# Kernel optimization log

Hardware: AMD Instinct MI355X
Metric: run time of the kernel (lower is better)

Reference implementation:

```python
import jax, jax.numpy as jnp
import numpy as np

D = 768
H = 12
DH = D // H  # 64


def setup_inputs() -> dict:
    key = jax.random.key(0)
    ks = jax.random.split(key, 7)
    B, N = 16, 1024
    sequences = jax.random.normal(ks[0], (B, N, D), dtype=jnp.float32)
    s = 1.0 / np.sqrt(DH)
    # per-head torch Linear params: weight [out, in] = [DH, DH], bias [DH]
    Wq = jax.random.uniform(ks[1], (H, DH, DH), jnp.float32, -s, s)
    Wk = jax.random.uniform(ks[2], (H, DH, DH), jnp.float32, -s, s)
    Wv = jax.random.uniform(ks[3], (H, DH, DH), jnp.float32, -s, s)
    bq = jax.random.uniform(ks[4], (H, DH), jnp.float32, -s, s)
    bk = jax.random.uniform(ks[5], (H, DH), jnp.float32, -s, s)
    bv = jax.random.uniform(ks[6], (H, DH), jnp.float32, -s, s)
    return {"sequences": sequences, "Wq": Wq, "Wk": Wk, "Wv": Wv,
            "bq": bq, "bk": bk, "bv": bv}


def reference(sequences, Wq, Wk, Wv, bq, bk, bv):
    B, N, _ = sequences.shape
    x = sequences.reshape(B, N, H, DH)  # head slices of the feature dim
    # torch Linear: y = x @ W.T + b  -> einsum over the 'in' axis of W
    q = jnp.einsum('bnhd,hed->bnhe', x, Wq) + bq
    k = jnp.einsum('bnhd,hed->bnhe', x, Wk) + bk
    v = jnp.einsum('bnhd,hed->bnhe', x, Wv) + bv
    scores = jnp.einsum('bnhe,bmhe->bhnm', q, k) / jnp.sqrt(jnp.float32(DH))
    attn = jax.nn.softmax(scores, axis=-1)  # [B,H,N,N]
    out = jnp.einsum('bhnm,bmhe->bnhe', attn, v)
    return out.reshape(B, N, H * DH)  # hstack of per-head outputs
```

## Files before the change

### kernel.cpp

```cpp
#include <hip/hip_runtime.h>


#define NH 12
#define DHEAD 64
#define BB 16
#define NSEQ 1024
#define DMODEL 768
#define LSTR 72
#define QSCALE 0.18033688f

typedef unsigned short u16;
typedef unsigned int u32;
typedef u16 u16x8 __attribute__((ext_vector_type(8)));
typedef u16 u16x4 __attribute__((ext_vector_type(4)));
typedef __bf16 bf16x8 __attribute__((ext_vector_type(8)));
typedef __bf16 bf16x2 __attribute__((ext_vector_type(2)));
typedef float f32x4 __attribute__((ext_vector_type(4)));
typedef int i32x2 __attribute__((ext_vector_type(2)));

union Frag { u16x8 u; bf16x8 b; u32 w[4]; };

__device__ __forceinline__ float fast_exp2(float x) {
#if __has_builtin(__builtin_amdgcn_exp2f)
    return __builtin_amdgcn_exp2f(x);
#else
    return exp2f(x);
#endif
}

__device__ __forceinline__ u16 f2bf(float f) {
    union { __bf16 h; u16 u; } c; c.h = (__bf16)f; return c.u;
}

__device__ __forceinline__ u32 pk2(float lo, float hi) {
    union { bf16x2 b; u32 u; } c;
    c.b[0] = (__bf16)lo; c.b[1] = (__bf16)hi;
    return c.u;
}

__device__ __forceinline__ u16x8 cvt8(const float* __restrict__ p) {
    f32x4 a = *(const f32x4*)p;
    f32x4 b = *(const f32x4*)(p + 4);
    Frag r;
    r.b[0] = (__bf16)a[0]; r.b[1] = (__bf16)a[1]; r.b[2] = (__bf16)a[2]; r.b[3] = (__bf16)a[3];
    r.b[4] = (__bf16)b[0]; r.b[5] = (__bf16)b[1]; r.b[6] = (__bf16)b[2]; r.b[7] = (__bf16)b[3];
    return r.u;
}

__device__ __forceinline__ int sw(int row, int slot) {
    return (row << 6) + (((slot + row) & 7) << 3);
}

__device__ __forceinline__ void lane4_shuffle(u32 a0, u32 a1, u32& wlo, u32& whi) {
    i32x2 t = __builtin_amdgcn_permlane32_swap((int)a0, (int)a1, false, false);
    i32x2 r = __builtin_amdgcn_permlane16_swap(t[0], t[1], false, false);
    wlo = (u32)r[0]; whi = (u32)r[1];
}

__global__ __launch_bounds__(256) void wcvt_kernel(
    const float* __restrict__ Wq, const float* __restrict__ Wk,
    const float* __restrict__ Wv, u16* __restrict__ Wb)
{
    const int bx = blockIdx.x;
    const int m = bx / 24;
    const int off = (bx % 24) * 2048 + threadIdx.x * 8;
    const float* srcs[3] = { Wq, Wk, Wv };
    *(u16x8*)(Wb + m * 49152 + off) = cvt8(srcs[m] + off);
}

__global__ __launch_bounds__(256) void kv_kernel(
    const float* __restrict__ x,
    const u16*  __restrict__ Wb,
    const float* __restrict__ bk, const float* __restrict__ bv,
    u16* __restrict__ Ko,
    u16* __restrict__ Vt)
{
    __shared__ __align__(16) u16 w_lds[2][64 * LSTR];
    __shared__ __align__(16) u16 x_lds[128 * LSTR];

    const int bid = blockIdx.x;
    const int h     = bid % NH;
    const int chunk = (bid / NH) & 7;
    const int b     = bid / (NH * 8);

    const int t = threadIdx.x, lane = t & 63, wave = t >> 6;
    const int qd = lane >> 4, lm = lane & 15;

    {
        const int row = t >> 2, d0 = (t & 3) * 16;
#pragma unroll
        for (int m = 0; m < 2; m++) {
            const u16* s = Wb + (1 + m) * 49152 + h * 4096 + row * 64 + d0;
            *(u16x8*)&w_lds[m][row * LSTR + d0]     = *(const u16x8*)s;
            *(u16x8*)&w_lds[m][row * LSTR + d0 + 8] = *(const u16x8*)(s + 8);
        }
        const int xr = t >> 1, xd = (t & 1) * 32;
        const float* s = x + ((size_t)(b * NSEQ + chunk * 128 + xr)) * DMODEL + h * DHEAD + xd;
#pragma unroll
        for (int i = 0; i < 4; i++)
            *(u16x8*)&x_lds[xr * LSTR + xd + i * 8] = cvt8(s + i * 8);
    }
    __syncthreads();

    Frag xfrag[2][2];
#pragma unroll
    for (int mt = 0; mt < 2; mt++)
#pragma unroll
        for (int kk = 0; kk < 2; kk++)
            xfrag[mt][kk].u = *(const u16x8*)&x_lds[(wave * 32 + mt * 16 + lm) * LSTR + kk * 32 + qd * 8];

    u16* tx = &x_lds[wave * 32 * LSTR];
    const int key_base = chunk * 128 + wave * 32;

#pragma unroll
    for (int et = 0; et < 4; et++) {
        Frag wfrag[2];
#pragma unroll
        for (int kk = 0; kk < 2; kk++)
            wfrag[kk].u = *(const u16x8*)&w_lds[0][(et * 16 + lm) * LSTR + kk * 32 + qd * 8];
        f32x4 acc0 = {0.f,0.f,0.f,0.f}, acc1 = {0.f,0.f,0.f,0.f};
#pragma unroll
        for (int kk = 0; kk < 2; kk++) {
            acc0 = __builtin_amdgcn_mfma_f32_16x16x32_bf16(wfrag[kk].b, xfrag[0][kk].b, acc0, 0, 0, 0);
            acc1 = __builtin_amdgcn_mfma_f32_16x16x32_bf16(wfrag[kk].b, xfrag[1][kk].b, acc1, 0, 0, 0);
        }
        f32x4 b4 = *(const f32x4*)&bk[h * DHEAD + et * 16 + qd * 4];
        u16x4 o0, o1;
#pragma unroll
        for (int r = 0; r < 4; r++) {
            o0[r] = f2bf(acc0[r] + b4[r]);
            o1[r] = f2bf(acc1[r] + b4[r]);
        }
        *(u16x4*)&tx[lm * LSTR + et * 16 + qd * 4]        = o0;
        *(u16x4*)&tx[(16 + lm) * LSTR + et * 16 + qd * 4] = o1;
    }
    {
        const size_t base_out = ((size_t)(b * NH + h) * NSEQ + key_base) * DHEAD;
#pragma unroll
        for (int j = 0; j < 4; j++) {
            const int row = j * 8 + (lane >> 3), col = (lane & 7) * 8;
            u16x8 v = *(const u16x8*)&tx[row * LSTR + col];
            *(u16x8*)(Ko + base_out + (size_t)row * DHEAD + col) = v;
        }
    }

    const size_t vt_base = ((size_t)(b * NH + h)) * DHEAD * NSEQ;
#pragma unroll
    for (int et = 0; et < 4; et++) {
        Frag wvfrag[2];
#pragma unroll
        for (int kk = 0; kk < 2; kk++)
            wvfrag[kk].u = *(const u16x8*)&w_lds[1][(et * 16 + lm) * LSTR + kk * 32 + qd * 8];
        const float bvv = bv[h * DHEAD + et * 16 + lm];
#pragma unroll
        for (int mt = 0; mt < 2; mt++) {
            f32x4 acc = {0.f,0.f,0.f,0.f};
#pragma unroll
            for (int kk = 0; kk < 2; kk++)
                acc = __builtin_amdgcn_mfma_f32_16x16x32_bf16(xfrag[mt][kk].b, wvfrag[kk].b, acc, 0, 0, 0);
            u16x4 o;
#pragma unroll
            for (int r = 0; r < 4; r++) o[r] = f2bf(acc[r] + bvv);
            *(u16x4*)(Vt + vt_base + (size_t)(et * 16 + lm) * NSEQ + key_base + mt * 16 + qd * 4) = o;
        }
    }
}

__global__ __launch_bounds__(512, 2) void attn_kernel(
    const float* __restrict__ x, const u16* __restrict__ Wb,
    const float* __restrict__ bq,
    const u16* __restrict__ K, const u16* __restrict__ Vt,
    float* __restrict__ out)
{
    __shared__ __align__(16) u16 k_lds[2][64 * 64];
    __shared__ __align__(16) u16 v_lds[2][64 * 64];

    const int bid = blockIdx.x;
    const int bh = bid % 192;
    const int qt = bid / 192;
    const int h = bh % NH, b = bh / NH;

    const int t = threadIdx.x, lane = t & 63, wave = t >> 6;
    const int qd = lane >> 4, lm = lane & 15;
    const size_t bh_off = (size_t)bh * NSEQ * DHEAD;
    const int tb = qt * 256;

    const u16* kb = K  + bh_off;
    const u16* vb = Vt + bh_off;

    const int srow = t >> 3, sc = t & 7;

    {
        const u16* wq = Wb + h * 4096 + srow * 64 + sc * 8;
        *(u16x8*)&k_lds[0][sw(srow, sc)] = *(const u16x8*)wq;
    }

    u16x8 kreg, vreg;
    kreg = *(const u16x8*)(kb + (size_t)srow * DHEAD + sc * 8);
    vreg = *(const u16x8*)(vb + (size_t)srow * NSEQ + sc * 8);
    __syncthreads();

    Frag qfrag[2][2];
#pragma unroll
    for (int mtl = 0; mtl < 2; mtl++) {
        const float* xs = x + ((size_t)(b * NSEQ + tb + wave * 32 + mtl * 16 + lm)) * DMODEL
                          + h * DHEAD + qd * 8;
        Frag xB[2];
        xB[0].u = cvt8(xs);
        xB[1].u = cvt8(xs + 32);
        u32 Ap[4], Bp[4];
#pragma unroll
        for (int et = 0; et < 4; et++) {
            Frag wqA[2];
#pragma unroll
            for (int kk = 0; kk < 2; kk++)
                wqA[kk].u = *(const u16x8*)&k_lds[0][sw(et * 16 + lm, kk * 4 + qd)];
            f32x4 acc = {0.f,0.f,0.f,0.f};
#pragma unroll
            for (int kk = 0; kk < 2; kk++)
                acc = __builtin_amdgcn_mfma_f32_16x16x32_bf16(wqA[kk].b, xB[kk].b, acc, 0, 0, 0);
            f32x4 b4 = *(const f32x4*)&bq[h * DHEAD + et * 16 + qd * 4];
            Ap[et] = pk2((acc[0] + b4[0]) * QSCALE, (acc[1] + b4[1]) * QSCALE);
            Bp[et] = pk2((acc[2] + b4[2]) * QSCALE, (acc[3] + b4[3]) * QSCALE);
        }
#pragma unroll
        for (int kk = 0; kk < 2; kk++) {
            lane4_shuffle(Ap[2 * kk], Ap[2 * kk + 1], qfrag[mtl][kk].w[0], qfrag[mtl][kk].w[2]);
            lane4_shuffle(Bp[2 * kk], Bp[2 * kk + 1], qfrag[mtl][kk].w[1], qfrag[mtl][kk].w[3]);
        }
    }

    *(u16x8*)&k_lds[1][sw(srow, sc)] = kreg;
    *(u16x8*)&v_lds[1][sw(srow, sc)] = vreg;
    kreg = *(const u16x8*)(kb + (size_t)(64 + srow) * DHEAD + sc * 8);
    vreg = *(const u16x8*)(vb + (size_t)srow * NSEQ + 64 + sc * 8);
    __syncthreads();

    f32x4 o_acc[2][4] = {};
    float rsum[2] = { 0.f, 0.f };

#pragma unroll 1
    for (int it = 0; it < NSEQ / 64; it++) {
        const int cur = 1 - (it & 1);

        if (it < NSEQ / 64 - 1) {
            *(u16x8*)&k_lds[1 - cur][sw(srow, sc)] = kreg;
            *(u16x8*)&v_lds[1 - cur][sw(srow, sc)] = vreg;
        }
        if (it < NSEQ / 64 - 2) {
            kreg = *(const u16x8*)(kb + (size_t)((it + 2) * 64 + srow) * DHEAD + sc * 8);
            vreg = *(const u16x8*)(vb + (size_t)srow * NSEQ + (it + 2) * 64 + sc * 8);
        }

        Frag kfrag[4][2];
#pragma unroll
        for (int kt = 0; kt < 4; kt++)
#pragma unroll
            for (int kk = 0; kk < 2; kk++)
                kfrag[kt][kk].u = *(const u16x8*)&k_lds[cur][sw(kt * 16 + lm, kk * 4 + qd)];

        Frag pfrag[2][2];
#pragma unroll
        for (int mt = 0; mt < 2; mt++) {
            f32x4 st[4];
            __builtin_amdgcn_s_setprio(1);
#pragma unroll
            for (int kt = 0; kt < 4; kt++) {
                f32x4 a = {0.f,0.f,0.f,0.f};
                a = __builtin_amdgcn_mfma_f32_16x16x32_bf16(kfrag[kt][0].b, qfrag[mt][0].b, a, 0, 0, 0);
                a = __builtin_amdgcn_mfma_f32_16x16x32_bf16(kfrag[kt][1].b, qfrag[mt][1].b, a, 0, 0, 0);
                st[kt] = a;
            }
            __builtin_amdgcn_s_setprio(0);
            float rs = 0.f;
            u32 Ap[4], Bp[4];
#pragma unroll
            for (int kt = 0; kt < 4; kt++) {
                float e0 = fast_exp2(st[kt][0]);
                float e1 = fast_exp2(st[kt][1]);
                float e2 = fast_exp2(st[kt][2]);
                float e3 = fast_exp2(st[kt][3]);
                rs += (e0 + e1) + (e2 + e3);
                Ap[kt] = pk2(e0, e1); Bp[kt] = pk2(e2, e3);
            }
            rsum[mt] += rs;
#pragma unroll
            for (int kk = 0; kk < 2; kk++) {
                lane4_shuffle(Ap[2 * kk], Ap[2 * kk + 1], pfrag[mt][kk].w[0], pfrag[mt][kk].w[2]);
                lane4_shuffle(Bp[2 * kk], Bp[2 * kk + 1], pfrag[mt][kk].w[1], pfrag[mt][kk].w[3]);
            }
        }

        __builtin_amdgcn_s_setprio(1);
#pragma unroll
        for (int dt = 0; dt < 4; dt++) {
            Frag vfrag[2];
#pragma unroll
            for (int kk = 0; kk < 2; kk++)
                vfrag[kk].u = *(const u16x8*)&v_lds[cur][sw(dt * 16 + lm, kk * 4 + qd)];
#pragma unroll
            for (int kk = 0; kk < 2; kk++)
#pragma unroll
                for (int mt = 0; mt < 2; mt++)
                    o_acc[mt][dt] = __builtin_amdgcn_mfma_f32_16x16x32_bf16(pfrag[mt][kk].b, vfrag[kk].b, o_acc[mt][dt], 0, 0, 0);
        }
        __builtin_amdgcn_s_setprio(0);

        __syncthreads();
    }

#pragma unroll
    for (int mt = 0; mt < 2; mt++) {
        float s = rsum[mt];
        s += __shfl_xor(s, 16);
        s += __shfl_xor(s, 32);
        float inv = 1.f / s;
        float inv4[4];
#pragma unroll
        for (int r = 0; r < 4; r++) inv4[r] = __shfl(inv, qd * 4 + r);
#pragma unroll
        for (int dt = 0; dt < 4; dt++) {
            const int e = dt * 16 + lm;
#pragma unroll
            for (int r = 0; r < 4; r++) {
                const int n_tok = tb + wave * 32 + mt * 16 + qd * 4 + r;
                out[((size_t)(b * NSEQ + n_tok)) * DMODEL + h * DHEAD + e] =
                    o_acc[mt][dt][r] * inv4[r];
            }
        }
    }
}

extern "C" void kernel_launch(void* const* d_in, const int* in_sizes, int n_in,
                              void* d_out, int out_size, void* d_ws, size_t ws_size,
                              hipStream_t stream) {
    const float* x  = (const float*)d_in[0];
    const float* Wq = (const float*)d_in[1];
    const float* Wk = (const float*)d_in[2];
    const float* Wv = (const float*)d_in[3];
    const float* bq = (const float*)d_in[4];
    const float* bk = (const float*)d_in[5];
    const float* bv = (const float*)d_in[6];
    float* out = (float*)d_out;

    const size_t KV_ELEMS = (size_t)BB * NH * NSEQ * DHEAD;
    u16* Kw  = (u16*)d_ws;
    u16* Vtw = Kw + KV_ELEMS;
    u16* Wb  = Vtw + KV_ELEMS;

    wcvt_kernel<<<72, 256, 0, stream>>>(Wq, Wk, Wv, Wb);
    kv_kernel<<<BB * 8 * NH, 256, 0, stream>>>(x, Wb, bk, bv, Kw, Vtw);
    attn_kernel<<<(NSEQ / 256) * BB * NH, 512, 0, stream>>>(x, Wb, bq, Kw, Vtw, out);
}
```

Before: 92.52 us.

## Fold weight conversion into consumers and process 128-key stages per barrier

```diff
diff --git a/kernel.cpp b/kernel.cpp
--- a/kernel.cpp
+++ b/kernel.cpp
@@ -57,20 +57,9 @@
     wlo = (u32)r[0]; whi = (u32)r[1];
 }
 
-__global__ __launch_bounds__(256) void wcvt_kernel(
-    const float* __restrict__ Wq, const float* __restrict__ Wk,
-    const float* __restrict__ Wv, u16* __restrict__ Wb)
-{
-    const int bx = blockIdx.x;
-    const int m = bx / 24;
-    const int off = (bx % 24) * 2048 + threadIdx.x * 8;
-    const float* srcs[3] = { Wq, Wk, Wv };
-    *(u16x8*)(Wb + m * 49152 + off) = cvt8(srcs[m] + off);
-}
-
 __global__ __launch_bounds__(256) void kv_kernel(
     const float* __restrict__ x,
-    const u16*  __restrict__ Wb,
+    const float* __restrict__ Wk, const float* __restrict__ Wv,
     const float* __restrict__ bk, const float* __restrict__ bv,
     u16* __restrict__ Ko,
     u16* __restrict__ Vt)
@@ -88,11 +77,12 @@
 
     {
         const int row = t >> 2, d0 = (t & 3) * 16;
+        const float* wsrc[2] = { Wk, Wv };
 #pragma unroll
         for (int m = 0; m < 2; m++) {
-            const u16* s = Wb + (1 + m) * 49152 + h * 4096 + row * 64 + d0;
-            *(u16x8*)&w_lds[m][row * LSTR + d0]     = *(const u16x8*)s;
-            *(u16x8*)&w_lds[m][row * LSTR + d0 + 8] = *(const u16x8*)(s + 8);
+            const float* s = wsrc[m] + h * 4096 + row * 64 + d0;
+            *(u16x8*)&w_lds[m][row * LSTR + d0]     = cvt8(s);
+            *(u16x8*)&w_lds[m][row * LSTR + d0 + 8] = cvt8(s + 8);
         }
         const int xr = t >> 1, xd = (t & 1) * 32;
         const float* s = x + ((size_t)(b * NSEQ + chunk * 128 + xr)) * DMODEL + h * DHEAD + xd;
@@ -167,13 +157,13 @@
 }
 
 __global__ __launch_bounds__(512, 2) void attn_kernel(
-    const float* __restrict__ x, const u16* __restrict__ Wb,
+    const float* __restrict__ x, const float* __restrict__ Wq,
     const float* __restrict__ bq,
     const u16* __restrict__ K, const u16* __restrict__ Vt,
     float* __restrict__ out)
 {
-    __shared__ __align__(16) u16 k_lds[2][64 * 64];
-    __shared__ __align__(16) u16 v_lds[2][64 * 64];
+    __shared__ __align__(16) u16 k_lds[2][2][64 * 64];
+    __shared__ __align__(16) u16 v_lds[2][2][64 * 64];
 
     const int bid = blockIdx.x;
     const int bh = bid % 192;
@@ -190,14 +180,14 @@
 
     const int srow = t >> 3, sc = t & 7;
 
-    {
-        const u16* wq = Wb + h * 4096 + srow * 64 + sc * 8;
-        *(u16x8*)&k_lds[0][sw(srow, sc)] = *(const u16x8*)wq;
-    }
-
-    u16x8 kreg, vreg;
-    kreg = *(const u16x8*)(kb + (size_t)srow * DHEAD + sc * 8);
-    vreg = *(const u16x8*)(vb + (size_t)srow * NSEQ + sc * 8);
+    *(u16x8*)&k_lds[0][0][sw(srow, sc)] = cvt8(Wq + h * 4096 + srow * 64 + sc * 8);
+
+    u16x8 kreg[2], vreg[2];
+#pragma unroll
+    for (int s = 0; s < 2; s++) {
+        kreg[s] = *(const u16x8*)(kb + (size_t)(s * 64 + srow) * DHEAD + sc * 8);
+        vreg[s] = *(const u16x8*)(vb + (size_t)srow * NSEQ + s * 64 + sc * 8);
+    }
     __syncthreads();
 
     Frag qfrag[2][2];
@@ -214,7 +204,7 @@
             Frag wqA[2];
 #pragma unroll
             for (int kk = 0; kk < 2; kk++)
-                wqA[kk].u = *(const u16x8*)&k_lds[0][sw(et * 16 + lm, kk * 4 + qd)];
+                wqA[kk].u = *(const u16x8*)&k_lds[0][0][sw(et * 16 + lm, kk * 4 + qd)];
             f32x4 acc = {0.f,0.f,0.f,0.f};
 #pragma unroll
             for (int kk = 0; kk < 2; kk++)
@@ -230,81 +220,93 @@
         }
     }
 
-    *(u16x8*)&k_lds[1][sw(srow, sc)] = kreg;
-    *(u16x8*)&v_lds[1][sw(srow, sc)] = vreg;
-    kreg = *(const u16x8*)(kb + (size_t)(64 + srow) * DHEAD + sc * 8);
-    vreg = *(const u16x8*)(vb + (size_t)srow * NSEQ + 64 + sc * 8);
+#pragma unroll
+    for (int s = 0; s < 2; s++) {
+        *(u16x8*)&k_lds[1][s][sw(srow, sc)] = kreg[s];
+        *(u16x8*)&v_lds[1][s][sw(srow, sc)] = vreg[s];
+        kreg[s] = *(const u16x8*)(kb + (size_t)(128 + s * 64 + srow) * DHEAD + sc * 8);
+        vreg[s] = *(const u16x8*)(vb + (size_t)srow * NSEQ + 128 + s * 64 + sc * 8);
+    }
     __syncthreads();
 
     f32x4 o_acc[2][4] = {};
     float rsum[2] = { 0.f, 0.f };
 
 #pragma unroll 1
-    for (int it = 0; it < NSEQ / 64; it++) {
-        const int cur = 1 - (it & 1);
-
-        if (it < NSEQ / 64 - 1) {
-            *(u16x8*)&k_lds[1 - cur][sw(srow, sc)] = kreg;
-            *(u16x8*)&v_lds[1 - cur][sw(srow, sc)] = vreg;
-        }
-        if (it < NSEQ / 64 - 2) {
-            kreg = *(const u16x8*)(kb + (size_t)((it + 2) * 64 + srow) * DHEAD + sc * 8);
-            vreg = *(const u16x8*)(vb + (size_t)srow * NSEQ + (it + 2) * 64 + sc * 8);
-        }
-
-        Frag kfrag[4][2];
-#pragma unroll
-        for (int kt = 0; kt < 4; kt++)
-#pragma unroll
-            for (int kk = 0; kk < 2; kk++)
-                kfrag[kt][kk].u = *(const u16x8*)&k_lds[cur][sw(kt * 16 + lm, kk * 4 + qd)];
-
-        Frag pfrag[2][2];
-#pragma unroll
-        for (int mt = 0; mt < 2; mt++) {
-            f32x4 st[4];
+    for (int itp = 0; itp < NSEQ / 128; itp++) {
+        const int cur = 1 - (itp & 1);
+
+        if (itp < NSEQ / 128 - 1) {
+#pragma unroll
+            for (int s = 0; s < 2; s++) {
+                *(u16x8*)&k_lds[1 - cur][s][sw(srow, sc)] = kreg[s];
+                *(u16x8*)&v_lds[1 - cur][s][sw(srow, sc)] = vreg[s];
+            }
+        }
+        if (itp < NSEQ / 128 - 2) {
+#pragma unroll
+            for (int s = 0; s < 2; s++) {
+                kreg[s] = *(const u16x8*)(kb + (size_t)((itp + 2) * 128 + s * 64 + srow) * DHEAD + sc * 8);
+                vreg[s] = *(const u16x8*)(vb + (size_t)srow * NSEQ + (itp + 2) * 128 + s * 64 + sc * 8);
+            }
+        }
+
+#pragma unroll
+        for (int s = 0; s < 2; s++) {
+            Frag kfrag[4][2];
+#pragma unroll
+            for (int kt = 0; kt < 4; kt++)
+#pragma unroll
+                for (int kk = 0; kk < 2; kk++)
+                    kfrag[kt][kk].u = *(const u16x8*)&k_lds[cur][s][sw(kt * 16 + lm, kk * 4 + qd)];
+
+            Frag pfrag[2][2];
+#pragma unroll
+            for (int mt = 0; mt < 2; mt++) {
+                f32x4 st[4];
+                __builtin_amdgcn_s_setprio(1);
+#pragma unroll
+                for (int kt = 0; kt < 4; kt++) {
+                    f32x4 a = {0.f,0.f,0.f,0.f};
+                    a = __builtin_amdgcn_mfma_f32_16x16x32_bf16(kfrag[kt][0].b, qfrag[mt][0].b, a, 0, 0, 0);
+                    a = __builtin_amdgcn_mfma_f32_16x16x32_bf16(kfrag[kt][1].b, qfrag[mt][1].b, a, 0, 0, 0);
+                    st[kt] = a;
+                }
+                __builtin_amdgcn_s_setprio(0);
+                float rs = 0.f;
+                u32 Ap[4], Bp[4];
+#pragma unroll
+                for (int kt = 0; kt < 4; kt++) {
+                    float e0 = fast_exp2(st[kt][0]);
+                    float e1 = fast_exp2(st[kt][1]);
+                    float e2 = fast_exp2(st[kt][2]);
+                    float e3 = fast_exp2(st[kt][3]);
+                    rs += (e0 + e1) + (e2 + e3);
+                    Ap[kt] = pk2(e0, e1); Bp[kt] = pk2(e2, e3);
+                }
+                rsum[mt] += rs;
+#pragma unroll
+                for (int kk = 0; kk < 2; kk++) {
+                    lane4_shuffle(Ap[2 * kk], Ap[2 * kk + 1], pfrag[mt][kk].w[0], pfrag[mt][kk].w[2]);
+                    lane4_shuffle(Bp[2 * kk], Bp[2 * kk + 1], pfrag[mt][kk].w[1], pfrag[mt][kk].w[3]);
+                }
+            }
+
             __builtin_amdgcn_s_setprio(1);
 #pragma unroll
-            for (int kt = 0; kt < 4; kt++) {
-                f32x4 a = {0.f,0.f,0.f,0.f};
-                a = __builtin_amdgcn_mfma_f32_16x16x32_bf16(kfrag[kt][0].b, qfrag[mt][0].b, a, 0, 0, 0);
-                a = __builtin_amdgcn_mfma_f32_16x16x32_bf16(kfrag[kt][1].b, qfrag[mt][1].b, a, 0, 0, 0);
-                st[kt] = a;
+            for (int dt = 0; dt < 4; dt++) {
+                Frag vfrag[2];
+#pragma unroll
+                for (int kk = 0; kk < 2; kk++)
+                    vfrag[kk].u = *(const u16x8*)&v_lds[cur][s][sw(dt * 16 + lm, kk * 4 + qd)];
+#pragma unroll
+                for (int kk = 0; kk < 2; kk++)
+#pragma unroll
+                    for (int mt = 0; mt < 2; mt++)
+                        o_acc[mt][dt] = __builtin_amdgcn_mfma_f32_16x16x32_bf16(pfrag[mt][kk].b, vfrag[kk].b, o_acc[mt][dt], 0, 0, 0);
             }
             __builtin_amdgcn_s_setprio(0);
-            float rs = 0.f;
-            u32 Ap[4], Bp[4];
-#pragma unroll
-            for (int kt = 0; kt < 4; kt++) {
-                float e0 = fast_exp2(st[kt][0]);
-                float e1 = fast_exp2(st[kt][1]);
-                float e2 = fast_exp2(st[kt][2]);
-                float e3 = fast_exp2(st[kt][3]);
-                rs += (e0 + e1) + (e2 + e3);
-                Ap[kt] = pk2(e0, e1); Bp[kt] = pk2(e2, e3);
-            }
-            rsum[mt] += rs;
-#pragma unroll
-            for (int kk = 0; kk < 2; kk++) {
-                lane4_shuffle(Ap[2 * kk], Ap[2 * kk + 1], pfrag[mt][kk].w[0], pfrag[mt][kk].w[2]);
-                lane4_shuffle(Bp[2 * kk], Bp[2 * kk + 1], pfrag[mt][kk].w[1], pfrag[mt][kk].w[3]);
-            }
-        }
-
-        __builtin_amdgcn_s_setprio(1);
-#pragma unroll
-        for (int dt = 0; dt < 4; dt++) {
-            Frag vfrag[2];
-#pragma unroll
-            for (int kk = 0; kk < 2; kk++)
-                vfrag[kk].u = *(const u16x8*)&v_lds[cur][sw(dt * 16 + lm, kk * 4 + qd)];
-#pragma unroll
-            for (int kk = 0; kk < 2; kk++)
-#pragma unroll
-                for (int mt = 0; mt < 2; mt++)
-                    o_acc[mt][dt] = __builtin_amdgcn_mfma_f32_16x16x32_bf16(pfrag[mt][kk].b, vfrag[kk].b, o_acc[mt][dt], 0, 0, 0);
-        }
-        __builtin_amdgcn_s_setprio(0);
+        }
 
         __syncthreads();
     }
@@ -346,9 +348,7 @@
     const size_t KV_ELEMS = (size_t)BB * NH * NSEQ * DHEAD;
     u16* Kw  = (u16*)d_ws;
     u16* Vtw = Kw + KV_ELEMS;
-    u16* Wb  = Vtw + KV_ELEMS;
-
-    wcvt_kernel<<<72, 256, 0, stream>>>(Wq, Wk, Wv, Wb);
-    kv_kernel<<<BB * 8 * NH, 256, 0, stream>>>(x, Wb, bk, bv, Kw, Vtw);
-    attn_kernel<<<(NSEQ / 256) * BB * NH, 512, 0, stream>>>(x, Wb, bq, Kw, Vtw, out);
-}
+
+    kv_kernel<<<BB * 8 * NH, 256, 0, stream>>>(x, Wk, Wv, bk, bv, Kw, Vtw);
+    attn_kernel<<<(NSEQ / 256) * BB * NH, 512, 0, stream>>>(x, Wq, bq, Kw, Vtw, out);
+}
```

Result: slower. 100.9 us (+9.0%).
